# Optimization experiments

Measured on AMD Instinct MI355X. Metric: run time of the kernel, lower is better.

Reference implementation:

```python
import jax, jax.numpy as jnp
import numpy as np

SEQ, NV, NH, NR = 32768, 256, 512, 256


def _bern(key, p):
    # torch.bernoulli: sample is non-differentiable
    return (jax.random.uniform(key, p.shape, dtype=p.dtype) < p).astype(p.dtype)


def setup_inputs() -> dict:
    key = jax.random.key(0)
    ks = jax.random.split(key, 8)
    f32 = jnp.float32
    return {
        "v_seq": (jax.random.uniform(ks[0], (SEQ, NV), dtype=f32) < 0.1).astype(f32),
        "W1": jax.random.normal(ks[1], (NV, NH), dtype=f32) * 0.01,
        "bv": jnp.zeros((NV,), f32),
        "bh1": jnp.zeros((NH,), f32),
        "W2": jax.random.normal(ks[2], (NH, NH), dtype=f32) * 0.01,
        "bh2": jnp.zeros((NH,), f32),
        "Wyv": jax.random.normal(ks[3], (NV, NR), dtype=f32) * 1e-4,
        "Wyh1": jax.random.normal(ks[4], (NH, NR), dtype=f32) * 1e-4,
        "Wyh2": jax.random.normal(ks[5], (NH, NR), dtype=f32) * 1e-4,
        "Wvu": jax.random.normal(ks[6], (NV, NR), dtype=f32) * 0.01,
        "Wuu": jax.random.normal(ks[7], (NR, NR), dtype=f32) * 0.01,
        "bu": jnp.zeros((NR,), f32),
        "k": 5,
    }


def reference(v_seq, W1, bv, bh1, W2, bh2, Wyv, Wyh1, Wyh2, Wvu, Wuu, bu, k):
    dtype = v_seq.dtype
    nr = Wuu.shape[0]
    seq_len = v_seq.shape[0]

    # vanilla tanh RNN (abstract _run_rnn in base class)
    def rnn_step(u, v):
        u_new = jnp.tanh(v @ Wvu + u @ Wuu + bu)
        return u_new, u_new

    _, rnn_out = jax.lax.scan(rnn_step, jnp.zeros((nr,), dtype), v_seq)
    shifted = jnp.concatenate([jnp.zeros((1, nr), dtype), rnn_out[:-1]], axis=0)

    bv_t = bv + shifted @ Wyv.T    # [S, NV]
    bh1_t = bh1 + shifted @ Wyh1.T  # [S, NH]
    bh2_t = bh2 + shifted @ Wyh2.T  # [S, NH]

    key = jax.random.key(42)

    # CD-k Gibbs chain, RBM1 (visible <-> hidden1)
    v_sample = v_seq
    mean_v = None
    for _ in range(k):
        key, k1, k2 = jax.random.split(key, 3)
        h = _bern(k1, jax.nn.sigmoid(v_sample @ W1 + bh1_t))
        mean_v = jax.nn.sigmoid(h @ W1.T + bv_t)
        v_sample = _bern(k2, mean_v)

    def free_energy1(v):
        return -(v * bv_t).sum(-1) - jax.nn.softplus(v @ W1 + bh1_t).sum(-1)

    cost1 = (free_energy1(v_seq) - free_energy1(jax.lax.stop_gradient(v_sample))).mean()

    # CD-k Gibbs chain, RBM2 (hidden1 <-> hidden2)
    h1 = jax.nn.sigmoid(v_seq @ W1 + bh1_t)
    h1_sample = h1
    for _ in range(k):
        key, k1, k2 = jax.random.split(key, 3)
        h2 = _bern(k1, jax.nn.sigmoid(h1_sample @ W2 + bh2_t))
        h1_sample = _bern(k2, jax.nn.sigmoid(h2 @ W2.T + bh1_t))

    def free_energy2(h):
        return -(h * bh1_t).sum(-1) - jax.nn.softplus(h @ W2 + bh2_t).sum(-1)

    cost2 = (free_energy2(h1) - free_energy2(jax.lax.stop_gradient(h1_sample))).mean()

    eps = 1e-10
    monitor = (v_seq * jnp.log(mean_v + eps)
               + (1.0 - v_seq) * jnp.log(1.0 - mean_v + eps)).sum() / seq_len
    return (cost1 + cost2, monitor)
```

## Files before the change

kernel.cpp:

```cpp
#include <hip/hip_runtime.h>
#include <cstdint>

#define S_LEN 32768
#define NV 256
#define NH 512
#define NR 256

typedef short bf16x8 __attribute__((ext_vector_type(8)));
typedef float f32x4 __attribute__((ext_vector_type(4)));
typedef unsigned short ushort_t;

__device__ __forceinline__ float b2f(ushort_t u) {
  return __uint_as_float(((uint32_t)u) << 16);
}
__device__ __forceinline__ ushort_t f2b(float f) {
  uint32_t x = __float_as_uint(f);
  uint32_t r = (x + 0x7fffu + ((x >> 16) & 1u)) >> 16;
  return (ushort_t)r;
}

#define GLOAD_LDS16(gsrc, ldst)                                        \
  __builtin_amdgcn_global_load_lds(                                    \
      (const __attribute__((address_space(1))) void*)(gsrc),           \
      (__attribute__((address_space(3))) void*)(ldst), 16, 0, 0)

#define TFR(x0,x1,r) { x0 += x1; x1 = ((x1 << (r)) | (x1 >> (32 - (r)))); x1 ^= x0; }
__host__ __forceinline__ void tf2x32(uint32_t k0, uint32_t k1,
                                     uint32_t x0, uint32_t x1,
                                     uint32_t* o0, uint32_t* o1) {
  uint32_t k2 = k0 ^ k1 ^ 0x1BD11BDAu;
  x0 += k0; x1 += k1;
  TFR(x0,x1,13) TFR(x0,x1,15) TFR(x0,x1,26) TFR(x0,x1,6)
  x0 += k1; x1 += k2 + 1u;
  TFR(x0,x1,17) TFR(x0,x1,29) TFR(x0,x1,16) TFR(x0,x1,24)
  x0 += k2; x1 += k0 + 2u;
  TFR(x0,x1,13) TFR(x0,x1,15) TFR(x0,x1,26) TFR(x0,x1,6)
  x0 += k0; x1 += k1 + 3u;
  TFR(x0,x1,17) TFR(x0,x1,29) TFR(x0,x1,16) TFR(x0,x1,24)
  x0 += k1; x1 += k2 + 4u;
  TFR(x0,x1,13) TFR(x0,x1,15) TFR(x0,x1,26) TFR(x0,x1,6)
  x0 += k2; x1 += k0 + 5u;
  *o0 = x0; *o1 = x1;
}

__device__ __forceinline__ uint32_t fast_hash(uint32_t k0, uint32_t k1, uint32_t idx) {
  uint32_t h = idx ^ k0;
  h *= 0xCC9E2D51u; h = (h << 15) | (h >> 17); h *= 0x1B873593u;
  h ^= k1;
  h ^= h >> 16; h *= 0x85EBCA6Bu;
  h ^= h >> 13; h *= 0xC2B2AE35u;
  h ^= h >> 16;
  return h;
}

__device__ __forceinline__ float wave_reduce(float v) {
#pragma unroll
  for (int o = 32; o > 0; o >>= 1) v += __shfl_down(v, o, 64);
  return v;
}
__device__ __forceinline__ float softplusf(float z) {
  return fmaxf(z, 0.f) + log1pf(expf(-fabsf(z)));
}

#define F_SAMP  4
#define F_H1    8
#define F_FE    16
#define F_MON   32
#define F_DOTB  64
#define F_DOTS  128

struct GemmArgs {
  const ushort_t* A;
  const ushort_t* BT;
  const ushort_t* Ax;
  const ushort_t* BXT;
  const float* bvec;
  int boff;
  ushort_t* C;
  ushort_t* C2;
  const float* vseqf;
  double* fe_acc;
  double* mon_acc;
  float sign;
  uint32_t rk0, rk1;
  int N, K, nbx;
};

template<int FLAGS>
__device__ __forceinline__ void run_gemm(const GemmArgs& g,
                                         const ushort_t* __restrict__ biasm, int ldb,
                                         ushort_t* __restrict__ As0,
                                         ushort_t* __restrict__ As1,
                                         ushort_t* __restrict__ Bs0,
                                         ushort_t* __restrict__ Bs1) {
  const int tid = threadIdx.x;
  const int lane = tid & 63, wave = tid >> 6;
  const int wm = wave >> 1, wn = wave & 1;
  const int q = lane >> 4, l16 = lane & 15;
  const int m0 = blockIdx.y * 128, n0 = blockIdx.x * 128;
  const int N = g.N, K = g.K;
  const int KT = K + 256;

  f32x4 acc[4][4];
#pragma unroll
  for (int mt = 0; mt < 4; mt++)
#pragma unroll
    for (int nt = 0; nt < 4; nt++) acc[mt][nt] = (f32x4){0.f, 0.f, 0.f, 0.f};

  auto stage = [&](ushort_t* As, ushort_t* Bs, int kks) {
    const ushort_t* Ap; const ushort_t* Bp; size_t lda, ldbt; int k0;
    if (kks < K) { Ap = g.A;  Bp = g.BT;  lda = (size_t)K; ldbt = (size_t)K; k0 = kks; }
    else         { Ap = g.Ax; Bp = g.BXT; lda = 256;       ldbt = 256;       k0 = kks - K; }
#pragma unroll
    for (int j = 0; j < 4; j++) {
      int c = j * 256 + tid;
      int r = c >> 3, bl = c & 7, bg = bl ^ (r & 7);
      const int ldso = (j * 256 + wave * 64) * 8;
      GLOAD_LDS16(&Ap[(size_t)(m0 + r) * lda + k0 + bg * 8], &As[ldso]);
      GLOAD_LDS16(&Bp[(size_t)(n0 + r) * ldbt + k0 + bg * 8], &Bs[ldso]);
    }
  };
  auto compute = [&](const ushort_t* As, const ushort_t* Bs) {
#pragma unroll
    for (int c = 0; c < 2; c++) {
      bf16x8 af[4], bf[4];
#pragma unroll
      for (int mt = 0; mt < 4; mt++) {
        int r = wm * 64 + mt * 16 + l16;
        af[mt] = *(const bf16x8*)&As[r * 64 + (((c * 4 + q) ^ (r & 7)) * 8)];
      }
#pragma unroll
      for (int nt = 0; nt < 4; nt++) {
        int r = wn * 64 + nt * 16 + l16;
        bf[nt] = *(const bf16x8*)&Bs[r * 64 + (((c * 4 + q) ^ (r & 7)) * 8)];
      }
#pragma unroll
      for (int mt = 0; mt < 4; mt++)
#pragma unroll
        for (int nt = 0; nt < 4; nt++)
          acc[mt][nt] = __builtin_amdgcn_mfma_f32_16x16x32_bf16(
              af[mt], bf[nt], acc[mt][nt], 0, 0, 0);
    }
  };

  stage(As0, Bs0, 0);
  __syncthreads();
  for (int kk = 0; kk < KT; kk += 128) {
    stage(As1, Bs1, kk + 64);
    compute(As0, Bs0);
    __syncthreads();
    if (kk + 128 < KT) stage(As0, Bs0, kk + 128);
    compute(As1, Bs1);
    __syncthreads();
  }

  float fe_sum = 0.f, mon_sum = 0.f;
#pragma unroll
  for (int mt = 0; mt < 4; mt++) {
#pragma unroll
    for (int nt = 0; nt < 4; nt++) {
      const int gn = n0 + wn * 64 + nt * 16 + l16;
      const int gmb = m0 + wm * 64 + mt * 16 + q * 4;
      const float bvv = g.bvec[gn];
      uint32_t h0 = 0, h1 = 0;
      if constexpr (FLAGS & F_SAMP) {
        uint32_t pb = (uint32_t)((gmb >> 1) * N + gn);
        h0 = fast_hash(g.rk0, g.rk1, pb);
        h1 = fast_hash(g.rk0, g.rk1, pb + (uint32_t)N);
      }
#pragma unroll
      for (int rg = 0; rg < 4; rg++) {
        const int gm = gmb + rg;
        const size_t idx = (size_t)gm * N + gn;
        float z = acc[mt][nt][rg] + bvv;
        float be = 0.f;
        if constexpr (FLAGS & (F_DOTB | F_DOTS))
          be = b2f(biasm[(size_t)gm * ldb + g.boff + gn]);
        if constexpr (FLAGS & (F_SAMP | F_H1 | F_MON)) {
          float e = __expf(-z);
          if constexpr (FLAGS & F_SAMP) {
            uint32_t hb = (rg & 2) ? h1 : h0;
            uint32_t ub = (rg & 1) ? (hb >> 16) : (hb & 0xffffu);
            float uu = (float)ub * (1.0f / 65536.0f);
            bool sbit = fmaf(uu, e, uu) < 1.f;
            g.C[idx] = sbit ? (ushort_t)0x3f80 : (ushort_t)0;
            if constexpr (FLAGS & F_DOTS) fe_sum += sbit ? be : 0.f;
          }
          if constexpr (FLAGS & (F_H1 | F_MON)) {
            float pp = __builtin_amdgcn_rcpf(1.f + e);
            if constexpr (FLAGS & F_H1) g.C2[idx] = f2b(pp);
            if constexpr (FLAGS & F_DOTB) fe_sum += pp * be;
            if constexpr (FLAGS & F_MON) {
              float v = g.vseqf[idx];
              mon_sum += (v != 0.f) ? logf(pp + 1e-10f) : logf(1.f - pp + 1e-10f);
            }
          }
        }
        if constexpr (FLAGS & F_FE) fe_sum += softplusf(z);
      }
    }
  }
  if constexpr (FLAGS & (F_FE | F_DOTB | F_DOTS)) {
    float s = wave_reduce(fe_sum);
    if (lane == 0) atomicAdd(g.fe_acc, (double)(-g.sign * s));
  }
  if constexpr (FLAGS & F_MON) {
    float s = wave_reduce(mon_sum);
    if (lane == 0) atomicAdd(g.mon_acc, (double)s);
  }
}

template<int FLAGS>
__global__ __launch_bounds__(256)
void gemm_samp(GemmArgs g, const ushort_t* __restrict__ biasm, int ldb) {
  __shared__ ushort_t As0[128 * 64], As1[128 * 64];
  __shared__ ushort_t Bs0[128 * 64], Bs1[128 * 64];
  if ((int)blockIdx.x >= g.nbx) return;
  run_gemm<FLAGS>(g, biasm, ldb, As0, As1, Bs0, Bs1);
}

template<int F0, int F1>
__global__ __launch_bounds__(256)
void gemm_pair(GemmArgs g0, GemmArgs g1, const ushort_t* __restrict__ biasm, int ldb) {
  __shared__ ushort_t As0[128 * 64], As1[128 * 64];
  __shared__ ushort_t Bs0[128 * 64], Bs1[128 * 64];
  if (blockIdx.z == 0) {
    if ((int)blockIdx.x >= g0.nbx) return;
    run_gemm<F0>(g0, biasm, ldb, As0, As1, Bs0, Bs1);
  } else {
    if ((int)blockIdx.x >= g1.nbx) return;
    run_gemm<F1>(g1, biasm, ldb, As0, As1, Bs0, Bs1);
  }
}

template<bool OUTF32, bool VDOT>
__global__ __launch_bounds__(256)
void gemm_bias(const ushort_t* __restrict__ A, const ushort_t* __restrict__ BT,
               const float* __restrict__ biasv, ushort_t* __restrict__ Cb,
               float* __restrict__ Cf, const float* __restrict__ vdata,
               double* __restrict__ dacc, int M, int N, int K) {
  __shared__ ushort_t As0[128 * 64], As1[128 * 64];
  __shared__ ushort_t Bs0[128 * 64], Bs1[128 * 64];
  const int tid = threadIdx.x;
  const int lane = tid & 63, wave = tid >> 6;
  const int wm = wave >> 1, wn = wave & 1;
  const int q = lane >> 4, l16 = lane & 15;
  const int m0 = blockIdx.y * 128, n0 = blockIdx.x * 128;

  f32x4 acc[4][4];
#pragma unroll
  for (int i = 0; i < 4; i++)
#pragma unroll
    for (int j = 0; j < 4; j++) acc[i][j] = (f32x4){0.f, 0.f, 0.f, 0.f};

  auto stage = [&](ushort_t* As, ushort_t* Bs, int kk) {
#pragma unroll
    for (int j = 0; j < 4; j++) {
      int c = j * 256 + tid;
      int r = c >> 3, bl = c & 7, bg = bl ^ (r & 7);
      const int ldso = (j * 256 + wave * 64) * 8;
      GLOAD_LDS16(&A[(size_t)(m0 + r) * K + kk + bg * 8], &As[ldso]);
      GLOAD_LDS16(&BT[(size_t)(n0 + r) * K + kk + bg * 8], &Bs[ldso]);
    }
  };
  auto compute = [&](const ushort_t* As, const ushort_t* Bs) {
#pragma unroll
    for (int c = 0; c < 2; c++) {
      bf16x8 af[4], bf[4];
#pragma unroll
      for (int mt = 0; mt < 4; mt++) {
        int r = wm * 64 + mt * 16 + l16;
        af[mt] = *(const bf16x8*)&As[r * 64 + (((c * 4 + q) ^ (r & 7)) * 8)];
      }
#pragma unroll
      for (int nt = 0; nt < 4; nt++) {
        int r = wn * 64 + nt * 16 + l16;
        bf[nt] = *(const bf16x8*)&Bs[r * 64 + (((c * 4 + q) ^ (r & 7)) * 8)];
      }
#pragma unroll
      for (int mt = 0; mt < 4; mt++)
#pragma unroll
        for (int nt = 0; nt < 4; nt++)
          acc[mt][nt] = __builtin_amdgcn_mfma_f32_16x16x32_bf16(
              af[mt], bf[nt], acc[mt][nt], 0, 0, 0);
    }
  };

  stage(As0, Bs0, 0);
  __syncthreads();
  for (int kk = 0; kk < K; kk += 128) {
    stage(As1, Bs1, kk + 64);
    compute(As0, Bs0);
    __syncthreads();
    if (kk + 128 < K) stage(As0, Bs0, kk + 128);
    compute(As1, Bs1);
    __syncthreads();
  }

  float dsum = 0.f;
#pragma unroll
  for (int mt = 0; mt < 4; mt++)
#pragma unroll
    for (int nt = 0; nt < 4; nt++) {
      const int gn = n0 + wn * 64 + nt * 16 + l16;
      const int gmb = m0 + wm * 64 + mt * 16 + q * 4;
      const float bvv = biasv[gn];
#pragma unroll
      for (int rg = 0; rg < 4; rg++) {
        const size_t idx = (size_t)(gmb + rg) * N + gn;
        float z = acc[mt][nt][rg] + bvv;
        if constexpr (OUTF32) Cf[idx] = z; else Cb[idx] = f2b(z);
        if constexpr (VDOT)
          if (n0 < 256) dsum += z * vdata[(size_t)(gmb + rg) * 256 + gn];
      }
    }
  if constexpr (VDOT) {
    if (n0 < 256) {
      float s = wave_reduce(dsum);
      if ((tid & 63) == 0) atomicAdd(dacc, (double)(-s));
    }
  }
}

__global__ __launch_bounds__(1024, 1)
void rnn_scan(const float* __restrict__ Apre, const float* __restrict__ Wuu,
              ushort_t* __restrict__ shifted) {
  const int tid = threadIdx.x;
  const int j = tid >> 2;
  const int s = tid & 3;
  const int t_begin = blockIdx.x * 128;
  const int t_end = t_begin + 128;
  const int t0 = (t_begin >= 16) ? (t_begin - 16) : 0;

  float w[64];
#pragma unroll
  for (int i = 0; i < 64; i++) w[i] = Wuu[(size_t)(s * 64 + i) * 256 + j];

  __shared__ float u[2][280];
  __shared__ float asg[32 * 256];
  if (tid < 256) u[0][(tid >> 6) * 68 + (tid & 63)] = 0.f;
  if (blockIdx.x == 0 && s == 0) shifted[j] = 0;
  __syncthreads();

  const int jp = (j >> 6) * 68 + (j & 63);
  int p = 0;
  for (int tb = t0; tb < t_end; tb += 32) {
    int srow = tb + (tid >> 5);
    if (srow >= S_LEN) srow = S_LEN - 1;
    int scol = (tid & 31) * 8;
    float4 a0 = *(const float4*)&Apre[(size_t)srow * 256 + scol];
    float4 a1 = *(const float4*)&Apre[(size_t)srow * 256 + scol + 4];
    *(float4*)&asg[(tid >> 5) * 256 + scol] = a0;
    *(float4*)&asg[(tid >> 5) * 256 + scol + 4] = a1;
    __syncthreads();
#pragma unroll 1
    for (int i = 0; i < 32; i++) {
      const int t = tb + i;
      if (t >= t_end) break;
      float p0 = 0.f, p1 = 0.f, p2 = 0.f, p3 = 0.f;
#pragma unroll
      for (int qq = 0; qq < 64; qq += 4) {
        float4 uv = *(const float4*)&u[p][s * 68 + qq];
        p0 = fmaf(uv.x, w[qq + 0], p0);
        p1 = fmaf(uv.y, w[qq + 1], p1);
        p2 = fmaf(uv.z, w[qq + 2], p2);
        p3 = fmaf(uv.w, w[qq + 3], p3);
      }
      float ps = (p0 + p1) + (p2 + p3);
      ps += __shfl_xor(ps, 1, 64);
      ps += __shfl_xor(ps, 2, 64);
      float z = asg[i * 256 + j] + ps;
      float e = __expf(2.f * z);
      float unew = 1.f - 2.f * __builtin_amdgcn_rcpf(e + 1.f);
      if (s == 0) {
        u[1 - p][jp] = unew;
        if (t >= t_begin && (t + 1) < S_LEN)
          shifted[(size_t)(t + 1) * 256 + j] = f2b(unew);
      }
      __syncthreads();
      p ^= 1;
    }
  }
}

__global__ __launch_bounds__(256)
void prep_all(const float* __restrict__ v_seq, ushort_t* __restrict__ vseq_bf,
              const float* __restrict__ Wyv, const float* __restrict__ Wyh1,
              const float* __restrict__ Wyh2, ushort_t* __restrict__ Wycat,
              const float* __restrict__ W1, ushort_t* __restrict__ BTw1t,
              ushort_t* __restrict__ BTw1,
              const float* __restrict__ W2, ushort_t* __restrict__ BTw2t,
              ushort_t* __restrict__ BTw2,
              const float* __restrict__ Wvu, ushort_t* __restrict__ BTwvu,
              const float* __restrict__ bv, const float* __restrict__ bh1,
              const float* __restrict__ bh2, float* __restrict__ bveccat) {
  int b = blockIdx.x;
  const int tid = threadIdx.x;
  if (b < 32768) { int i = b * 256 + tid; vseq_bf[i] = f2b(v_seq[i]); return; }
  b -= 32768;
  if (b < 256)  { int i = b * 256 + tid; Wycat[i] = f2b(Wyv[i]); return; }
  b -= 256;
  if (b < 512)  { int i = b * 256 + tid; Wycat[65536 + i] = f2b(Wyh1[i]); return; }
  b -= 512;
  if (b < 512)  { int i = b * 256 + tid; Wycat[196608 + i] = f2b(Wyh2[i]); return; }
  b -= 512;
  if (b < 512)  { int i = b * 256 + tid; BTw1t[i] = f2b(W1[i]); return; }
  b -= 512;
  if (b < 1024) { int i = b * 256 + tid; BTw2t[i] = f2b(W2[i]); return; }
  b -= 1024;
  if (b < 256)  { int i = b * 256 + tid; int r = i >> 8, c = i & 255;
                  BTwvu[c * 256 + r] = f2b(Wvu[i]); return; }
  b -= 256;
  if (b < 512)  { int i = b * 256 + tid; int r = i >> 9, c = i & 511;
                  BTw1[(size_t)c * 256 + r] = f2b(W1[i]); return; }
  b -= 512;
  if (b < 1024) { int i = b * 256 + tid; int r = i >> 9, c = i & 511;
                  BTw2[(size_t)c * 512 + r] = f2b(W2[i]); return; }
  b -= 1024;
  { int i = b * 256 + tid;
    if (i < 1280)
      bveccat[i] = (i < 256) ? bv[i] : (i < 768) ? bh1[i - 256] : bh2[i - 768]; }
}

__global__ void finalize_kernel(const double* __restrict__ acc, float* __restrict__ out) {
  out[0] = (float)(acc[0] / (double)S_LEN);
  out[1] = (float)(acc[1] / (double)S_LEN);
}

extern "C" void kernel_launch(void* const* d_in, const int* in_sizes, int n_in,
                              void* d_out, int out_size, void* d_ws, size_t ws_size,
                              hipStream_t stream) {
  (void)in_sizes; (void)n_in; (void)out_size; (void)ws_size;
  const float* v_seq = (const float*)d_in[0];
  const float* W1    = (const float*)d_in[1];
  const float* bv    = (const float*)d_in[2];
  const float* bh1   = (const float*)d_in[3];
  const float* W2    = (const float*)d_in[4];
  const float* bh2   = (const float*)d_in[5];
  const float* Wyv   = (const float*)d_in[6];
  const float* Wyh1  = (const float*)d_in[7];
  const float* Wyh2  = (const float*)d_in[8];
  const float* Wvu   = (const float*)d_in[9];
  const float* Wuu   = (const float*)d_in[10];
  const float* bu    = (const float*)d_in[11];
  float* out = (float*)d_out;

  const size_t SN = (size_t)S_LEN * NV;
  const size_t SH = (size_t)S_LEN * NH;
  const int NB = NV + NH + NH;
  char* base = (char*)d_ws;
  size_t cur = 0;
  auto take = [&](size_t bytes) { size_t o = cur; cur += (bytes + 255) & ~(size_t)255; return o; };
  double*   acc      = (double*)  (base + take(64));
  ushort_t* BTwvu    = (ushort_t*)(base + take(65536 * 2));
  ushort_t* Wycat    = (ushort_t*)(base + take((size_t)NB * NR * 2));
  float*    bveccat  = (float*)   (base + take(NB * 4));
  ushort_t* BTw1     = (ushort_t*)(base + take(131072 * 2));
  ushort_t* BTw1t    = (ushort_t*)(base + take(131072 * 2));
  ushort_t* BTw2     = (ushort_t*)(base + take(262144 * 2));
  ushort_t* BTw2t    = (ushort_t*)(base + take(262144 * 2));
  ushort_t* vseq_bf  = (ushort_t*)(base + take(SN * 2));
  ushort_t* shifted  = (ushort_t*)(base + take(SN * 2));
  ushort_t* bias_cat = (ushort_t*)(base + take((size_t)S_LEN * NB * 2));
  ushort_t* h1buf    = (ushort_t*)(base + take(SH * 2));
  ushort_t* sampA    = (ushort_t*)(base + take(SH * 2));
  ushort_t* sampB    = (ushort_t*)(base + take(SN * 2));
  ushort_t* sampC    = (ushort_t*)(base + take(SH * 2));
  ushort_t* sampD = h1buf;
  float* Arnn = (float*)bias_cat;

  uint32_t ka[20], kb[20];
  uint32_t K0 = 0u, K1 = 42u;
  for (int it = 0; it < 10; it++) {
    uint32_t n0, n1, a0, a1, b0, b1;
    tf2x32(K0, K1, 0u, 0u, &n0, &n1);
    tf2x32(K0, K1, 0u, 1u, &a0, &a1);
    tf2x32(K0, K1, 0u, 2u, &b0, &b1);
    ka[2 * it] = a0; kb[2 * it] = a1;
    ka[2 * it + 1] = b0; kb[2 * it + 1] = b1;
    K0 = n0; K1 = n1;
  }

  hipMemsetAsync(acc, 0, 2 * sizeof(double), stream);

  dim3 blk(256);
  prep_all<<<dim3(37381), blk, 0, stream>>>(
      v_seq, vseq_bf, Wyv, Wyh1, Wyh2, Wycat, W1, BTw1t, BTw1,
      W2, BTw2t, BTw2, Wvu, BTwvu, bv, bh1, bh2, bveccat);

  const int M = S_LEN;
  gemm_bias<true, false><<<dim3(2, M / 128), blk, 0, stream>>>(
      vseq_bf, BTwvu, bu, nullptr, Arnn, nullptr, nullptr, M, NV, NV);
  rnn_scan<<<dim3(S_LEN / 128), dim3(1024), 0, stream>>>(Arnn, Wuu, shifted);
  gemm_bias<false, true><<<dim3(NB / 128, M / 128), blk, 0, stream>>>(
      shifted, Wycat, bveccat, bias_cat, nullptr, v_seq, acc, M, NB, NR);

  const int OFF_BV = 0, OFF_BH1 = NV, OFF_BH2 = NV + NH;
  auto mk = [&](const ushort_t* A, const ushort_t* BT, int boff, ushort_t* C,
                ushort_t* C2, const float* vs, float sign, int key, int N, int K) {
    GemmArgs g;
    g.A = A; g.BT = BT; g.boff = boff;
    g.Ax = shifted;
    g.BXT = Wycat + (size_t)boff * 256;
    g.bvec = bveccat + boff;
    g.C = C; g.C2 = C2; g.vseqf = vs;
    g.fe_acc = acc; g.mon_acc = acc + 1; g.sign = sign;
    g.rk0 = key >= 0 ? ka[key] : 0; g.rk1 = key >= 0 ? kb[key] : 0;
    g.N = N; g.K = K; g.nbx = N / 128;
    return g;
  };

  gemm_samp<F_SAMP | F_H1 | F_FE | F_DOTB>
      <<<dim3(4, M / 128), blk, 0, stream>>>(
      mk(vseq_bf, BTw1, OFF_BH1, sampA, h1buf, nullptr, 1.0f, 0, NH, NV),
      bias_cat, NB);

  dim3 pg(4, M / 128, 2);
  GemmArgs V[5], Hh[4], A2g[5], B2g[5];
  for (int it = 0; it < 5; it++) {
    if (it > 0)
      Hh[it - 1] = mk(sampB, BTw1, OFF_BH1, sampA, nullptr, nullptr, 0.f,
                      2 * it, NH, NV);
    V[it] = mk(sampA, BTw1t, OFF_BV, sampB, nullptr,
               (it == 4) ? v_seq : nullptr, (it == 4) ? -1.0f : 0.f,
               2 * it + 1, NV, NH);
    A2g[it] = mk((it == 0) ? h1buf : sampD,
                 BTw2, OFF_BH2, sampC, nullptr, nullptr,
                 (it == 0) ? 1.0f : 0.f, 10 + 2 * it, NH, NH);
    B2g[it] = mk(sampC, BTw2t, OFF_BH1, sampD, nullptr, nullptr,
                 (it == 4) ? -1.0f : 0.f, 11 + 2 * it, NH, NH);
  }
  GemmArgs FE1 = mk(sampB, BTw1, OFF_BH1, nullptr, nullptr, nullptr, -1.0f,
                    -1, NH, NV);
  GemmArgs FE2 = mk(sampD, BTw2, OFF_BH2, nullptr, nullptr, nullptr, -1.0f,
                    -1, NH, NH);

  gemm_pair<F_SAMP, F_SAMP | F_FE>
      <<<pg, blk, 0, stream>>>(V[0], A2g[0], bias_cat, NB);
  gemm_pair<F_SAMP, F_SAMP>
      <<<pg, blk, 0, stream>>>(Hh[0], B2g[0], bias_cat, NB);
  gemm_pair<F_SAMP, F_SAMP>
      <<<pg, blk, 0, stream>>>(V[1], A2g[1], bias_cat, NB);
  gemm_pair<F_SAMP, F_SAMP>
      <<<pg, blk, 0, stream>>>(Hh[1], B2g[1], bias_cat, NB);
  gemm_pair<F_SAMP, F_SAMP>
      <<<pg, blk, 0, stream>>>(V[2], A2g[2], bias_cat, NB);
  gemm_pair<F_SAMP, F_SAMP>
      <<<pg, blk, 0, stream>>>(Hh[2], B2g[2], bias_cat, NB);
  gemm_pair<F_SAMP, F_SAMP>
      <<<pg, blk, 0, stream>>>(V[3], A2g[3], bias_cat, NB);
  gemm_pair<F_SAMP, F_SAMP>
      <<<pg, blk, 0, stream>>>(Hh[3], B2g[3], bias_cat, NB);
  gemm_pair<F_SAMP | F_MON | F_DOTS, F_SAMP>
      <<<pg, blk, 0, stream>>>(V[4], A2g[4], bias_cat, NB);
  gemm_pair<F_FE, F_SAMP | F_DOTS>
      <<<pg, blk, 0, stream>>>(FE1, B2g[4], bias_cat, NB);

  gemm_samp<F_FE><<<dim3(4, M / 128), blk, 0, stream>>>(FE2, bias_cat, NB);

  finalize_kernel<<<1, 1, 0, stream>>>(acc, out);
}
```

Baseline: 1.453 ms.

## Drop precomputed bias matrix; accumulate per-step bias in separate MFMA accumulator

```diff
diff --git a/kernel.cpp b/kernel.cpp
--- a/kernel.cpp
+++ b/kernel.cpp
@@ -68,6 +68,7 @@
 #define F_MON   32
 #define F_DOTB  64
 #define F_DOTS  128
+#define F_DOTV  256
 
 struct GemmArgs {
   const ushort_t* A;
@@ -75,7 +76,6 @@
   const ushort_t* Ax;
   const ushort_t* BXT;
   const float* bvec;
-  int boff;
   ushort_t* C;
   ushort_t* C2;
   const float* vseqf;
@@ -86,41 +86,56 @@
   int N, K, nbx;
 };
 
+__device__ __forceinline__ void xcd_swz(int* bx, int* by) {
+  const int gx = (int)gridDim.x;
+  const int lin = (int)blockIdx.y * gx + (int)blockIdx.x;
+  const int cpx = (gx * (int)gridDim.y) >> 3;
+  const int w = (lin & 7) * cpx + (lin >> 3);
+  const int lg = 31 - __clz(gx);
+  *by = w >> lg;
+  *bx = w & (gx - 1);
+}
+
 template<int FLAGS>
-__device__ __forceinline__ void run_gemm(const GemmArgs& g,
-                                         const ushort_t* __restrict__ biasm, int ldb,
+__device__ __forceinline__ void run_gemm(const GemmArgs& g, int bx, int by,
                                          ushort_t* __restrict__ As0,
                                          ushort_t* __restrict__ As1,
                                          ushort_t* __restrict__ Bs0,
                                          ushort_t* __restrict__ Bs1) {
+  constexpr bool HASB = (FLAGS & (F_DOTB | F_DOTS | F_DOTV)) != 0;
   const int tid = threadIdx.x;
   const int lane = tid & 63, wave = tid >> 6;
   const int wm = wave >> 1, wn = wave & 1;
   const int q = lane >> 4, l16 = lane & 15;
-  const int m0 = blockIdx.y * 128, n0 = blockIdx.x * 128;
+  const int m0 = by * 128, n0 = bx * 128;
   const int N = g.N, K = g.K;
   const int KT = K + 256;
 
   f32x4 acc[4][4];
+  f32x4 accB[4][4];
 #pragma unroll
   for (int mt = 0; mt < 4; mt++)
 #pragma unroll
-    for (int nt = 0; nt < 4; nt++) acc[mt][nt] = (f32x4){0.f, 0.f, 0.f, 0.f};
+    for (int nt = 0; nt < 4; nt++) {
+      acc[mt][nt] = (f32x4){0.f, 0.f, 0.f, 0.f};
+      if constexpr (HASB) accB[mt][nt] = (f32x4){0.f, 0.f, 0.f, 0.f};
+    }
 
   auto stage = [&](ushort_t* As, ushort_t* Bs, int kks) {
-    const ushort_t* Ap; const ushort_t* Bp; size_t lda, ldbt; int k0;
-    if (kks < K) { Ap = g.A;  Bp = g.BT;  lda = (size_t)K; ldbt = (size_t)K; k0 = kks; }
-    else         { Ap = g.Ax; Bp = g.BXT; lda = 256;       ldbt = 256;       k0 = kks - K; }
+    const ushort_t* Ap; const ushort_t* Bp; size_t lda; int k0;
+    if (kks < K) { Ap = g.A;  Bp = g.BT;  lda = (size_t)K; k0 = kks; }
+    else         { Ap = g.Ax; Bp = g.BXT; lda = 256;       k0 = kks - K; }
 #pragma unroll
     for (int j = 0; j < 4; j++) {
       int c = j * 256 + tid;
       int r = c >> 3, bl = c & 7, bg = bl ^ (r & 7);
+      (void)bl;
       const int ldso = (j * 256 + wave * 64) * 8;
       GLOAD_LDS16(&Ap[(size_t)(m0 + r) * lda + k0 + bg * 8], &As[ldso]);
-      GLOAD_LDS16(&Bp[(size_t)(n0 + r) * ldbt + k0 + bg * 8], &Bs[ldso]);
+      GLOAD_LDS16(&Bp[(size_t)(n0 + r) * lda + k0 + bg * 8], &Bs[ldso]);
     }
   };
-  auto compute = [&](const ushort_t* As, const ushort_t* Bs) {
+  auto compute_into = [&](f32x4 (&ac)[4][4], const ushort_t* As, const ushort_t* Bs) {
 #pragma unroll
     for (int c = 0; c < 2; c++) {
       bf16x8 af[4], bf[4];
@@ -138,8 +153,8 @@
       for (int mt = 0; mt < 4; mt++)
 #pragma unroll
         for (int nt = 0; nt < 4; nt++)
-          acc[mt][nt] = __builtin_amdgcn_mfma_f32_16x16x32_bf16(
-              af[mt], bf[nt], acc[mt][nt], 0, 0, 0);
+          ac[mt][nt] = __builtin_amdgcn_mfma_f32_16x16x32_bf16(
+              af[mt], bf[nt], ac[mt][nt], 0, 0, 0);
     }
   };
 
@@ -147,10 +162,12 @@
   __syncthreads();
   for (int kk = 0; kk < KT; kk += 128) {
     stage(As1, Bs1, kk + 64);
-    compute(As0, Bs0);
+    if (HASB && kk >= K) compute_into(accB, As0, Bs0);
+    else                 compute_into(acc,  As0, Bs0);
     __syncthreads();
     if (kk + 128 < KT) stage(As0, Bs0, kk + 128);
-    compute(As1, Bs1);
+    if (HASB && (kk + 64) >= K) compute_into(accB, As1, Bs1);
+    else                        compute_into(acc,  As1, Bs1);
     __syncthreads();
   }
 
@@ -172,10 +189,14 @@
       for (int rg = 0; rg < 4; rg++) {
         const int gm = gmb + rg;
         const size_t idx = (size_t)gm * N + gn;
-        float z = acc[mt][nt][rg] + bvv;
-        float be = 0.f;
-        if constexpr (FLAGS & (F_DOTB | F_DOTS))
-          be = b2f(biasm[(size_t)gm * ldb + g.boff + gn]);
+        float z, be = 0.f;
+        if constexpr (HASB) {
+          be = accB[mt][nt][rg] + bvv;
+          z = acc[mt][nt][rg] + be;
+        } else {
+          z = acc[mt][nt][rg] + bvv;
+        }
+        if constexpr (FLAGS & F_DOTV) fe_sum += be * g.vseqf[idx];
         if constexpr (FLAGS & (F_SAMP | F_H1 | F_MON)) {
           float e = __expf(-z);
           if constexpr (FLAGS & F_SAMP) {
@@ -200,7 +221,7 @@
       }
     }
   }
-  if constexpr (FLAGS & (F_FE | F_DOTB | F_DOTS)) {
+  if constexpr (FLAGS & (F_FE | F_DOTB | F_DOTS | F_DOTV)) {
     float s = wave_reduce(fe_sum);
     if (lane == 0) atomicAdd(g.fe_acc, (double)(-g.sign * s));
   }
@@ -212,40 +233,45 @@
 
 template<int FLAGS>
 __global__ __launch_bounds__(256)
-void gemm_samp(GemmArgs g, const ushort_t* __restrict__ biasm, int ldb) {
+void gemm_samp(GemmArgs g) {
   __shared__ ushort_t As0[128 * 64], As1[128 * 64];
   __shared__ ushort_t Bs0[128 * 64], Bs1[128 * 64];
-  if ((int)blockIdx.x >= g.nbx) return;
-  run_gemm<FLAGS>(g, biasm, ldb, As0, As1, Bs0, Bs1);
+  int bx, by;
+  xcd_swz(&bx, &by);
+  if (bx >= g.nbx) return;
+  run_gemm<FLAGS>(g, bx, by, As0, As1, Bs0, Bs1);
 }
 
 template<int F0, int F1>
 __global__ __launch_bounds__(256)
-void gemm_pair(GemmArgs g0, GemmArgs g1, const ushort_t* __restrict__ biasm, int ldb) {
+void gemm_pair(GemmArgs g0, GemmArgs g1) {
   __shared__ ushort_t As0[128 * 64], As1[128 * 64];
   __shared__ ushort_t Bs0[128 * 64], Bs1[128 * 64];
+  int bx, by;
+  xcd_swz(&bx, &by);
   if (blockIdx.z == 0) {
-    if ((int)blockIdx.x >= g0.nbx) return;
-    run_gemm<F0>(g0, biasm, ldb, As0, As1, Bs0, Bs1);
+    if (bx >= g0.nbx) return;
+    run_gemm<F0>(g0, bx, by, As0, As1, Bs0, Bs1);
   } else {
-    if ((int)blockIdx.x >= g1.nbx) return;
-    run_gemm<F1>(g1, biasm, ldb, As0, As1, Bs0, Bs1);
-  }
-}
-
-template<bool OUTF32, bool VDOT>
+    if (bx >= g1.nbx) return;
+    run_gemm<F1>(g1, bx, by, As0, As1, Bs0, Bs1);
+  }
+}
+
 __global__ __launch_bounds__(256)
 void gemm_bias(const ushort_t* __restrict__ A, const ushort_t* __restrict__ BT,
-               const float* __restrict__ biasv, ushort_t* __restrict__ Cb,
-               float* __restrict__ Cf, const float* __restrict__ vdata,
-               double* __restrict__ dacc, int M, int N, int K) {
+               const float* __restrict__ biasv, float* __restrict__ Cf,
+               int M, int N, int K) {
   __shared__ ushort_t As0[128 * 64], As1[128 * 64];
   __shared__ ushort_t Bs0[128 * 64], Bs1[128 * 64];
   const int tid = threadIdx.x;
   const int lane = tid & 63, wave = tid >> 6;
   const int wm = wave >> 1, wn = wave & 1;
   const int q = lane >> 4, l16 = lane & 15;
-  const int m0 = blockIdx.y * 128, n0 = blockIdx.x * 128;
+  int bx, by;
+  xcd_swz(&bx, &by);
+  const int m0 = by * 128, n0 = bx * 128;
+  (void)lane;
 
   f32x4 acc[4][4];
 #pragma unroll
@@ -258,6 +284,7 @@
     for (int j = 0; j < 4; j++) {
       int c = j * 256 + tid;
       int r = c >> 3, bl = c & 7, bg = bl ^ (r & 7);
+      (void)bl;
       const int ldso = (j * 256 + wave * 64) * 8;
       GLOAD_LDS16(&A[(size_t)(m0 + r) * K + kk + bg * 8], &As[ldso]);
       GLOAD_LDS16(&BT[(size_t)(n0 + r) * K + kk + bg * 8], &Bs[ldso]);
@@ -297,7 +324,6 @@
     __syncthreads();
   }
 
-  float dsum = 0.f;
 #pragma unroll
   for (int mt = 0; mt < 4; mt++)
 #pragma unroll
@@ -306,20 +332,9 @@
       const int gmb = m0 + wm * 64 + mt * 16 + q * 4;
       const float bvv = biasv[gn];
 #pragma unroll
-      for (int rg = 0; rg < 4; rg++) {
-        const size_t idx = (size_t)(gmb + rg) * N + gn;
-        float z = acc[mt][nt][rg] + bvv;
-        if constexpr (OUTF32) Cf[idx] = z; else Cb[idx] = f2b(z);
-        if constexpr (VDOT)
-          if (n0 < 256) dsum += z * vdata[(size_t)(gmb + rg) * 256 + gn];
-      }
-    }
-  if constexpr (VDOT) {
-    if (n0 < 256) {
-      float s = wave_reduce(dsum);
-      if ((tid & 63) == 0) atomicAdd(dacc, (double)(-s));
-    }
-  }
+      for (int rg = 0; rg < 4; rg++)
+        Cf[(size_t)(gmb + rg) * N + gn] = acc[mt][nt][rg] + bvv;
+    }
 }
 
 __global__ __launch_bounds__(1024, 1)
@@ -447,27 +462,25 @@
 
   const size_t SN = (size_t)S_LEN * NV;
   const size_t SH = (size_t)S_LEN * NH;
-  const int NB = NV + NH + NH;
   char* base = (char*)d_ws;
   size_t cur = 0;
   auto take = [&](size_t bytes) { size_t o = cur; cur += (bytes + 255) & ~(size_t)255; return o; };
   double*   acc      = (double*)  (base + take(64));
   ushort_t* BTwvu    = (ushort_t*)(base + take(65536 * 2));
-  ushort_t* Wycat    = (ushort_t*)(base + take((size_t)NB * NR * 2));
-  float*    bveccat  = (float*)   (base + take(NB * 4));
+  ushort_t* Wycat    = (ushort_t*)(base + take((size_t)1280 * NR * 2));
+  float*    bveccat  = (float*)   (base + take(1280 * 4));
   ushort_t* BTw1     = (ushort_t*)(base + take(131072 * 2));
   ushort_t* BTw1t    = (ushort_t*)(base + take(131072 * 2));
   ushort_t* BTw2     = (ushort_t*)(base + take(262144 * 2));
   ushort_t* BTw2t    = (ushort_t*)(base + take(262144 * 2));
   ushort_t* vseq_bf  = (ushort_t*)(base + take(SN * 2));
   ushort_t* shifted  = (ushort_t*)(base + take(SN * 2));
-  ushort_t* bias_cat = (ushort_t*)(base + take((size_t)S_LEN * NB * 2));
+  float*    Arnn     = (float*)   (base + take(SN * 4));
   ushort_t* h1buf    = (ushort_t*)(base + take(SH * 2));
   ushort_t* sampA    = (ushort_t*)(base + take(SH * 2));
   ushort_t* sampB    = (ushort_t*)(base + take(SN * 2));
   ushort_t* sampC    = (ushort_t*)(base + take(SH * 2));
   ushort_t* sampD = h1buf;
-  float* Arnn = (float*)bias_cat;
 
   uint32_t ka[20], kb[20];
   uint32_t K0 = 0u, K1 = 42u;
@@ -489,17 +502,15 @@
       W2, BTw2t, BTw2, Wvu, BTwvu, bv, bh1, bh2, bveccat);
 
   const int M = S_LEN;
-  gemm_bias<true, false><<<dim3(2, M / 128), blk, 0, stream>>>(
-      vseq_bf, BTwvu, bu, nullptr, Arnn, nullptr, nullptr, M, NV, NV);
+  gemm_bias<<<dim3(2, M / 128), blk, 0, stream>>>(
+      vseq_bf, BTwvu, bu, Arnn, M, NV, NV);
   rnn_scan<<<dim3(S_LEN / 128), dim3(1024), 0, stream>>>(Arnn, Wuu, shifted);
-  gemm_bias<false, true><<<dim3(NB / 128, M / 128), blk, 0, stream>>>(
-      shifted, Wycat, bveccat, bias_cat, nullptr, v_seq, acc, M, NB, NR);
 
   const int OFF_BV = 0, OFF_BH1 = NV, OFF_BH2 = NV + NH;
   auto mk = [&](const ushort_t* A, const ushort_t* BT, int boff, ushort_t* C,
                 ushort_t* C2, const float* vs, float sign, int key, int N, int K) {
     GemmArgs g;
-    g.A = A; g.BT = BT; g.boff = boff;
+    g.A = A; g.BT = BT;
     g.Ax = shifted;
     g.BXT = Wycat + (size_t)boff * 256;
     g.bvec = bveccat + boff;
@@ -512,8 +523,7 @@
 
   gemm_samp<F_SAMP | F_H1 | F_FE | F_DOTB>
       <<<dim3(4, M / 128), blk, 0, stream>>>(
-      mk(vseq_bf, BTw1, OFF_BH1, sampA, h1buf, nullptr, 1.0f, 0, NH, NV),
-      bias_cat, NB);
+      mk(vseq_bf, BTw1, OFF_BH1, sampA, h1buf, nullptr, 1.0f, 0, NH, NV));
 
   dim3 pg(4, M / 128, 2);
   GemmArgs V[5], Hh[4], A2g[5], B2g[5];
@@ -522,7 +532,8 @@
       Hh[it - 1] = mk(sampB, BTw1, OFF_BH1, sampA, nullptr, nullptr, 0.f,
                       2 * it, NH, NV);
     V[it] = mk(sampA, BTw1t, OFF_BV, sampB, nullptr,
-               (it == 4) ? v_seq : nullptr, (it == 4) ? -1.0f : 0.f,
+               (it == 4 || it == 0) ? v_seq : nullptr,
+               (it == 4) ? -1.0f : (it == 0) ? 1.0f : 0.f,
                2 * it + 1, NV, NH);
     A2g[it] = mk((it == 0) ? h1buf : sampD,
                  BTw2, OFF_BH2, sampC, nullptr, nullptr,
@@ -535,28 +546,28 @@
   GemmArgs FE2 = mk(sampD, BTw2, OFF_BH2, nullptr, nullptr, nullptr, -1.0f,
                     -1, NH, NH);
 
-  gemm_pair<F_SAMP, F_SAMP | F_FE>
-      <<<pg, blk, 0, stream>>>(V[0], A2g[0], bias_cat, NB);
-  gemm_pair<F_SAMP, F_SAMP>
-      <<<pg, blk, 0, stream>>>(Hh[0], B2g[0], bias_cat, NB);
-  gemm_pair<F_SAMP, F_SAMP>
-      <<<pg, blk, 0, stream>>>(V[1], A2g[1], bias_cat, NB);
-  gemm_pair<F_SAMP, F_SAMP>
-      <<<pg, blk, 0, stream>>>(Hh[1], B2g[1], bias_cat, NB);
-  gemm_pair<F_SAMP, F_SAMP>
-      <<<pg, blk, 0, stream>>>(V[2], A2g[2], bias_cat, NB);
-  gemm_pair<F_SAMP, F_SAMP>
-      <<<pg, blk, 0, stream>>>(Hh[2], B2g[2], bias_cat, NB);
-  gemm_pair<F_SAMP, F_SAMP>
-      <<<pg, blk, 0, stream>>>(V[3], A2g[3], bias_cat, NB);
-  gemm_pair<F_SAMP, F_SAMP>
-      <<<pg, blk, 0, stream>>>(Hh[3], B2g[3], bias_cat, NB);
+  gemm_pair<F_SAMP | F_DOTV, F_SAMP | F_FE>
+      <<<pg, blk, 0, stream>>>(V[0], A2g[0]);
+  gemm_pair<F_SAMP, F_SAMP>
+      <<<pg, blk, 0, stream>>>(Hh[0], B2g[0]);
+  gemm_pair<F_SAMP, F_SAMP>
+      <<<pg, blk, 0, stream>>>(V[1], A2g[1]);
+  gemm_pair<F_SAMP, F_SAMP>
+      <<<pg, blk, 0, stream>>>(Hh[1], B2g[1]);
+  gemm_pair<F_SAMP, F_SAMP>
+      <<<pg, blk, 0, stream>>>(V[2], A2g[2]);
+  gemm_pair<F_SAMP, F_SAMP>
+      <<<pg, blk, 0, stream>>>(Hh[2], B2g[2]);
+  gemm_pair<F_SAMP, F_SAMP>
+      <<<pg, blk, 0, stream>>>(V[3], A2g[3]);
+  gemm_pair<F_SAMP, F_SAMP>
+      <<<pg, blk, 0, stream>>>(Hh[3], B2g[3]);
   gemm_pair<F_SAMP | F_MON | F_DOTS, F_SAMP>
-      <<<pg, blk, 0, stream>>>(V[4], A2g[4], bias_cat, NB);
+      <<<pg, blk, 0, stream>>>(V[4], A2g[4]);
   gemm_pair<F_FE, F_SAMP | F_DOTS>
-      <<<pg, blk, 0, stream>>>(FE1, B2g[4], bias_cat, NB);
-
-  gemm_samp<F_FE><<<dim3(4, M / 128), blk, 0, stream>>>(FE2, bias_cat, NB);
+      <<<pg, blk, 0, stream>>>(FE1, B2g[4]);
+
+  gemm_samp<F_FE><<<dim3(4, M / 128), blk, 0, stream>>>(FE2);
 
   finalize_kernel<<<1, 1, 0, stream>>>(acc, out);
 }
```

After: 1.429 ms. No clear change (-1.7%).
